# Kernel tuning notes

Measured on AMD Instinct MI355X. Metric: run time of the kernel, lower is better.

Reference implementation:

```python
import jax, jax.numpy as jnp
import numpy as np

N_NODES = 40000
IN_CH, HID_CH, OUT_CH = 128, 128, 64
N_EDGES = 640000
N_LABEL = 200000


def gcn_conv(x, edge_index, W, b):
    """PyG-style GCNConv: x' = D^{-1/2}(A+I)D^{-1/2} (x W) + b."""
    n = x.shape[0]
    loops = jnp.arange(n, dtype=edge_index.dtype)
    src = jnp.concatenate([edge_index[0], loops])  # [E+N]
    dst = jnp.concatenate([edge_index[1], loops])  # [E+N]
    deg = jax.ops.segment_sum(jnp.ones_like(dst, dtype=x.dtype), dst, num_segments=n)
    dinv = jnp.where(deg > 0, jax.lax.rsqrt(deg), 0.0)
    norm = dinv[src] * dinv[dst]                   # [E+N]
    h = x @ W                                      # [n, out]
    msg = h[src] * norm[:, None]                   # gather + scale
    agg = jax.ops.segment_sum(msg, dst, num_segments=n)
    return agg + b


def setup_inputs() -> dict:
    key = jax.random.key(0)
    k = jax.random.split(key, 8)
    x = jax.random.normal(k[0], (N_NODES, IN_CH), dtype=jnp.float32)
    edge_index = jax.random.randint(k[1], (2, N_EDGES), 0, N_NODES, dtype=jnp.int64)
    edge_label_index = jax.random.randint(k[2], (2, N_LABEL), 0, N_NODES, dtype=jnp.int64)
    s1 = 1.0 / np.sqrt(IN_CH)
    s2 = 1.0 / np.sqrt(HID_CH)
    W1 = jax.random.uniform(k[3], (IN_CH, HID_CH), jnp.float32, -s1, s1)
    b1 = jnp.zeros((HID_CH,), jnp.float32)
    W2 = jax.random.uniform(k[4], (HID_CH, OUT_CH), jnp.float32, -s2, s2)
    b2 = jnp.zeros((OUT_CH,), jnp.float32)
    return {"x": x, "edge_index": edge_index, "edge_label_index": edge_label_index,
            "W1": W1, "b1": b1, "W2": W2, "b2": b2}


def reference(x, edge_index, edge_label_index, W1, b1, W2, b2):
    # encode: conv1 -> relu -> conv2
    h = jax.nn.relu(gcn_conv(x, edge_index, W1, b1))
    z = gcn_conv(h, edge_index, W2, b2)            # [N, OUT_CH]
    # decode: dot-product score per candidate edge
    logits = jnp.sum(z[edge_label_index[0]] * z[edge_label_index[1]], axis=-1)
    return logits
```

## Files before the change

kernel.cpp:

```cpp
#include <hip/hip_runtime.h>
#include <hip/hip_bf16.h>

constexpr int IN_CH  = 128;
constexpr int HID_CH = 128;
constexpr int OUT_CH = 64;
constexpr int SCAN_CHUNK = 1024;

typedef __attribute__((ext_vector_type(8))) short bf16x8;
typedef __attribute__((ext_vector_type(4))) float f32x4;


__device__ inline unsigned short f2bf(float f) {
  __hip_bfloat16 h = __float2bfloat16(f);
  return *reinterpret_cast<unsigned short*>(&h);
}
__device__ inline unsigned pack_bf16x2(float lo, float hi) {
  return (unsigned)f2bf(lo) | ((unsigned)f2bf(hi) << 16);
}
__device__ inline float bf_lo(unsigned u) { return __uint_as_float(u << 16); }
__device__ inline float bf_hi(unsigned u) { return __uint_as_float(u & 0xffff0000u); }


__global__ __launch_bounds__(256) void k_zero(int* __restrict__ a, int n) {
  int i = (blockIdx.x * 256 + threadIdx.x) * 4;
  if (i + 3 < n) *(int4*)&a[i] = make_int4(0, 0, 0, 0);
  else for (int j = 0; j < 4 && i + j < n; ++j) a[i + j] = 0;
}


__global__ void k_count(const int* __restrict__ dst, int* __restrict__ cnt,
                        int* __restrict__ ord, int E) {
  int e = (blockIdx.x * blockDim.x + threadIdx.x) * 4;
  if (e + 3 < E) {
    int4 v = *(const int4*)&dst[e];
    int4 o;
    o.x = atomicAdd(&cnt[v.x], 1);
    o.y = atomicAdd(&cnt[v.y], 1);
    o.z = atomicAdd(&cnt[v.z], 1);
    o.w = atomicAdd(&cnt[v.w], 1);
    *(int4*)&ord[e] = o;
  } else {
    for (int j = 0; j < 4 && e + j < E; ++j) ord[e + j] = atomicAdd(&cnt[dst[e + j]], 1);
  }
}

__global__ __launch_bounds__(256) void k_scan_part(const int* __restrict__ cnt,
                                                   int* __restrict__ bsum,
                                                   float* __restrict__ dinv, int N) {
  int t = threadIdx.x;
  int base = blockIdx.x * SCAN_CHUNK + t * 4;
  int s = 0;
  if (base + 3 < N) {
    int4 v = *(const int4*)&cnt[base];
    s = v.x + v.y + v.z + v.w;
    float4 d;
    d.x = rsqrtf((float)v.x + 1.0f);
    d.y = rsqrtf((float)v.y + 1.0f);
    d.z = rsqrtf((float)v.z + 1.0f);
    d.w = rsqrtf((float)v.w + 1.0f);
    *(float4*)&dinv[base] = d;
  } else {
    for (int j = 0; j < 4; ++j)
      if (base + j < N) {
        int c = cnt[base + j];
        s += c;
        dinv[base + j] = rsqrtf((float)c + 1.0f);
      }
  }
  __shared__ int red[256];
  red[t] = s; __syncthreads();
  for (int off = 128; off; off >>= 1) {
    if (t < off) red[t] += red[t + off];
    __syncthreads();
  }
  if (t == 0) bsum[blockIdx.x] = red[0];
}

__global__ __launch_bounds__(256) void k_scan_fill(const int* __restrict__ cnt,
                                                   const int* __restrict__ bsum,
                                                   int* __restrict__ rowptr, int N, int E) {
  int t = threadIdx.x;
  int boff = 0;
  for (int i = 0; i < blockIdx.x; ++i) boff += bsum[i];
  int base = blockIdx.x * SCAN_CHUNK + t * 4;
  int v[4] = {0, 0, 0, 0};
  if (base + 3 < N) {
    int4 q = *(const int4*)&cnt[base];
    v[0] = q.x; v[1] = q.y; v[2] = q.z; v[3] = q.w;
  } else {
    for (int j = 0; j < 4; ++j) if (base + j < N) v[j] = cnt[base + j];
  }
  int mysum = v[0] + v[1] + v[2] + v[3];
  __shared__ int s[256];
  s[t] = mysum; __syncthreads();
  for (int off = 1; off < 256; off <<= 1) {
    int add = (t >= off) ? s[t - off] : 0;
    __syncthreads();
    s[t] += add;
    __syncthreads();
  }
  int run = boff + s[t] - mysum;
  for (int j = 0; j < 4; ++j) {
    if (base + j < N) rowptr[base + j] = run;
    run += v[j];
  }
  if (blockIdx.x == 0 && t == 0) rowptr[N] = E;
}

__global__ void k_fill(const int* __restrict__ src, const int* __restrict__ dst,
                       const int* __restrict__ ord, const int* __restrict__ rowptr,
                       int* __restrict__ col, int E) {
  int e0 = (blockIdx.x * blockDim.x + threadIdx.x) * 4;
  if (e0 >= E) return;
  if (e0 + 3 < E) {
    int4 sv = *(const int4*)&src[e0];
    int4 dv = *(const int4*)&dst[e0];
    int4 ov = *(const int4*)&ord[e0];
    col[rowptr[dv.x] + ov.x] = sv.x;
    col[rowptr[dv.y] + ov.y] = sv.y;
    col[rowptr[dv.z] + ov.z] = sv.z;
    col[rowptr[dv.w] + ov.w] = sv.w;
  } else {
    for (int j = 0; j < 4 && e0 + j < E; ++j)
      col[rowptr[dst[e0 + j]] + ord[e0 + j]] = src[e0 + j];
  }
}


template <int OUT, bool A_BF16>
__global__ __launch_bounds__(256) void k_gemm(const void* __restrict__ Xv,
                                              const float* __restrict__ W,
                                              const float* __restrict__ dinv,
                                              unsigned short* __restrict__ Y, int N) {
  constexpr int KD = 128;
  constexpr int NCG = OUT / 32;
  __shared__ unsigned short Wt[OUT * KD];
  int t = threadIdx.x;
  for (int i = t * 4; i < KD * OUT; i += 1024) {
    int k = i / OUT, c = i % OUT;
    float4 w4 = *(const float4*)&W[i];
    float wa[4] = {w4.x, w4.y, w4.z, w4.w};
#pragma unroll
    for (int j = 0; j < 4; ++j) {
      int colj = c + j;
      int byte = colj * (KD * 2) + k * 2;
      byte ^= ((colj & 7) << 4);
      *(unsigned short*)((char*)Wt + byte) = f2bf(wa[j]);
    }
  }
  __syncthreads();

  int w = t >> 6, l = t & 63;
  int lr = l & 15, kg = (l >> 4) * 8;
  int r = blockIdx.x * 64 + w * 16 + lr;
  bool valid = r < N;

  f32x4 acc[OUT / 16];
#pragma unroll
  for (int n = 0; n < OUT / 16; ++n) acc[n] = f32x4{0.f, 0.f, 0.f, 0.f};

#pragma unroll
  for (int kb = 0; kb < KD / 32; ++kb) {
    bf16x8 a = bf16x8{0, 0, 0, 0, 0, 0, 0, 0};
    if (valid) {
      if (A_BF16) {
        a = *(const bf16x8*)((const unsigned short*)Xv +
                             ((size_t)(kb >> 1) * N + r) * 64 + (kb & 1) * 32 + kg);
      } else {
        const float* xrow = (const float*)Xv + (size_t)r * KD + kb * 32 + kg;
        float4 x0 = *(const float4*)xrow;
        float4 x1 = *(const float4*)(xrow + 4);
        a[0] = (short)f2bf(x0.x); a[1] = (short)f2bf(x0.y);
        a[2] = (short)f2bf(x0.z); a[3] = (short)f2bf(x0.w);
        a[4] = (short)f2bf(x1.x); a[5] = (short)f2bf(x1.y);
        a[6] = (short)f2bf(x1.z); a[7] = (short)f2bf(x1.w);
      }
    }
#pragma unroll
    for (int n = 0; n < OUT / 16; ++n) {
      int col = n * 16 + lr;
      int byte = col * (KD * 2) + (kb * 32 + kg) * 2;
      byte ^= ((col & 7) << 4);
      bf16x8 b = *(const bf16x8*)((const char*)Wt + byte);
      acc[n] = __builtin_amdgcn_mfma_f32_16x16x32_bf16(a, b, acc[n], 0, 0, 0);
    }
  }

  int orow = blockIdx.x * 64 + w * 16 + (l >> 4) * 4;
  float dn[4];
#pragma unroll
  for (int i = 0; i < 4; ++i) dn[i] = (orow + i < N) ? dinv[orow + i] : 0.f;
#pragma unroll
  for (int i = 0; i < 4; ++i) {
    if (orow + i >= N) continue;
#pragma unroll
    for (int n = 0; n < OUT / 16; ++n)
      Y[((size_t)(n / NCG) * N + (orow + i)) * (OUT / 2) + (n % NCG) * 16 + lr] =
          f2bf(acc[n][i] * dn[i]);
  }
}


template <int CPU, bool RELU>
__global__ __launch_bounds__(256) void k_agg(const unsigned* __restrict__ T,
                                             const int* __restrict__ rowptr,
                                             const int* __restrict__ col,
                                             const float* __restrict__ dinv,
                                             const float* __restrict__ bias,
                                             unsigned* __restrict__ Out, int N) {
  constexpr int NPW = 64 / CPU;
  constexpr int NPB = 4 * NPW;
  int bid = blockIdx.x;
  int xcd = bid & 7, chunk = bid >> 3;
  int pass = xcd >> 2, sub = xcd & 3;
  int w = threadIdx.x >> 6, l = threadIdx.x & 63;
  int n = (chunk * 4 + sub) * NPB + w * NPW + l / CPU;
  if (n >= N) return;
  int cp = l % CPU;
  const unsigned* Tp = T + (size_t)pass * N * CPU;
  float dn = dinv[n];
  unsigned u0 = Tp[(size_t)n * CPU + cp];
  float ax = bf_lo(u0), ay = bf_hi(u0);
  int p = rowptr[n], pend = rowptr[n + 1];
  for (; p + 8 <= pend; p += 8) {
    int s[8]; unsigned g[8];
#pragma unroll
    for (int j = 0; j < 8; ++j) s[j] = __builtin_nontemporal_load(&col[p + j]);
#pragma unroll
    for (int j = 0; j < 8; ++j) g[j] = Tp[(size_t)s[j] * CPU + cp];
#pragma unroll
    for (int j = 0; j < 8; ++j) { ax += bf_lo(g[j]); ay += bf_hi(g[j]); }
  }
  if (p + 4 <= pend) {
    int s[4]; unsigned g[4];
#pragma unroll
    for (int j = 0; j < 4; ++j) s[j] = __builtin_nontemporal_load(&col[p + j]);
#pragma unroll
    for (int j = 0; j < 4; ++j) g[j] = Tp[(size_t)s[j] * CPU + cp];
#pragma unroll
    for (int j = 0; j < 4; ++j) { ax += bf_lo(g[j]); ay += bf_hi(g[j]); }
    p += 4;
  }
  for (; p < pend; ++p) {
    unsigned g = Tp[(size_t)__builtin_nontemporal_load(&col[p]) * CPU + cp];
    ax += bf_lo(g); ay += bf_hi(g);
  }
  float2 b2 = ((const float2*)bias)[pass * CPU + cp];
  float vx = dn * ax + b2.x, vy = dn * ay + b2.y;
  if (RELU) { vx = fmaxf(vx, 0.f); vy = fmaxf(vy, 0.f); }
  Out[(size_t)pass * N * CPU + (size_t)n * CPU + cp] = pack_bf16x2(vx, vy);
}


__global__ __launch_bounds__(256) void k_decode(const unsigned* __restrict__ Z,
                                                const int* __restrict__ ia,
                                                const int* __restrict__ ib,
                                                float* __restrict__ out, int N, int L) {
  int t = blockIdx.x * 256 + threadIdx.x;
  int i = t >> 3;
  if (i >= L) return;
  int e = t & 7;
  int a = ia[i], b = ib[i];
  size_t base = (size_t)(e >> 2) * N * 16 + (size_t)(e & 3) * 4;
  uint4 za = *(const uint4*)&Z[base + (size_t)a * 16];
  uint4 zb = *(const uint4*)&Z[base + (size_t)b * 16];
  float p = bf_lo(za.x) * bf_lo(zb.x) + bf_hi(za.x) * bf_hi(zb.x)
          + bf_lo(za.y) * bf_lo(zb.y) + bf_hi(za.y) * bf_hi(zb.y)
          + bf_lo(za.z) * bf_lo(zb.z) + bf_hi(za.z) * bf_hi(zb.z)
          + bf_lo(za.w) * bf_lo(zb.w) + bf_hi(za.w) * bf_hi(zb.w);
  p += __shfl_xor(p, 1);
  p += __shfl_xor(p, 2);
  p += __shfl_xor(p, 4);
  if (e == 0) out[i] = p;
}

extern "C" void kernel_launch(void* const* d_in, const int* in_sizes, int n_in,
                              void* d_out, int out_size, void* d_ws, size_t ws_size,
                              hipStream_t stream) {
  const float* x   = (const float*)d_in[0];
  const int*   ei  = (const int*)d_in[1];
  const int*   eli = (const int*)d_in[2];
  const float* W1  = (const float*)d_in[3];
  const float* b1  = (const float*)d_in[4];
  const float* W2  = (const float*)d_in[5];
  const float* b2  = (const float*)d_in[6];
  float* logits = (float*)d_out;

  int N = in_sizes[0] / IN_CH;
  int E = in_sizes[1] / 2;
  int L = in_sizes[2] / 2;
  const int* src = ei;
  const int* dst = ei + E;
  const int* la  = eli;
  const int* lb  = eli + L;

  char* ws = (char*)d_ws;
  size_t off = 0;
  auto alloc = [&](size_t bytes) {
    void* p = ws + off;
    off = (off + bytes + 255) & ~(size_t)255;
    return p;
  };
  int*      cnt    = (int*)alloc((size_t)N * 4);
  int*      rowptr = (int*)alloc((size_t)(N + 1) * 4);
  float*    dinv   = (float*)alloc((size_t)N * 4);
  int*      col    = (int*)alloc((size_t)E * 4);
  int*      ord    = (int*)alloc((size_t)E * 4);
  unsigned short* hsp  = (unsigned short*)alloc((size_t)N * HID_CH * 2);
  unsigned short* hrbp = (unsigned short*)alloc((size_t)N * HID_CH * 2);
  unsigned short* h2sp = (unsigned short*)alloc((size_t)N * OUT_CH * 2);
  unsigned short* zup  = (unsigned short*)alloc((size_t)N * OUT_CH * 2);
  int*      bsum   = (int*)alloc(256 * 4);

  const int TB = 256;
  int nscan = (N + SCAN_CHUNK - 1) / SCAN_CHUNK;
  k_zero<<<(N / 4 + TB - 1) / TB, TB, 0, stream>>>(cnt, N);
  k_count<<<(E / 4 + TB - 1) / TB, TB, 0, stream>>>(dst, cnt, ord, E);
  k_scan_part<<<nscan, 256, 0, stream>>>(cnt, bsum, dinv, N);
  k_scan_fill<<<nscan, 256, 0, stream>>>(cnt, bsum, rowptr, N, E);
  k_fill <<<(E / 4 + TB - 1) / TB, TB, 0, stream>>>(src, dst, ord, rowptr, col, E);

  k_gemm<HID_CH, false><<<(N + 63) / 64, 256, 0, stream>>>(x, W1, dinv, hsp, N);
  {
    int nchunk = (N + 8 * 4 - 1) / (8 * 4);
    k_agg<32, true><<<nchunk * 8, 256, 0, stream>>>(
        (const unsigned*)hsp, rowptr, col, dinv, b1, (unsigned*)hrbp, N);
  }

  k_gemm<OUT_CH, true><<<(N + 63) / 64, 256, 0, stream>>>(hrbp, W2, dinv, h2sp, N);
  {
    int nchunk = (N + 16 * 4 - 1) / (16 * 4);
    k_agg<16, false><<<nchunk * 8, 256, 0, stream>>>(
        (const unsigned*)h2sp, rowptr, col, dinv, b2, (unsigned*)zup, N);
  }

  k_decode<<<((size_t)L * 8 + 255) / 256, 256, 0, stream>>>(
      (const unsigned*)zup, la, lb, logits, N, L);
}
```

Baseline: 144.4 us.

## Split feature layout into 32-column slabs and make final embeddings row-contiguous

Layer-1 features now live in four 32-column bf16 slabs instead of two 64-column ones. Both aggregation kernels use 16 lanes per node, with passes spread across XCD-interleaved blocks, so each gathered row is a 64-byte segment. The second aggregation writes z row-contiguous with nontemporal stores, letting decode load one full 128-byte row per endpoint. This aims to improve per-XCD cache locality during gathers and to coalesce the decode reads, at the cost of more aggregation passes re-reading col/rowptr.

```diff
diff --git a/kernel.cpp b/kernel.cpp
--- a/kernel.cpp
+++ b/kernel.cpp
@@ -133,7 +133,6 @@
                                               const float* __restrict__ dinv,
                                               unsigned short* __restrict__ Y, int N) {
   constexpr int KD = 128;
-  constexpr int NCG = OUT / 32;
   __shared__ unsigned short Wt[OUT * KD];
   int t = threadIdx.x;
   for (int i = t * 4; i < KD * OUT; i += 1024) {
@@ -164,8 +163,7 @@
     bf16x8 a = bf16x8{0, 0, 0, 0, 0, 0, 0, 0};
     if (valid) {
       if (A_BF16) {
-        a = *(const bf16x8*)((const unsigned short*)Xv +
-                             ((size_t)(kb >> 1) * N + r) * 64 + (kb & 1) * 32 + kg);
+        a = *(const bf16x8*)((const unsigned short*)Xv + ((size_t)kb * N + r) * 32 + kg);
       } else {
         const float* xrow = (const float*)Xv + (size_t)r * KD + kb * 32 + kg;
         float4 x0 = *(const float4*)xrow;
@@ -195,31 +193,31 @@
     if (orow + i >= N) continue;
 #pragma unroll
     for (int n = 0; n < OUT / 16; ++n)
-      Y[((size_t)(n / NCG) * N + (orow + i)) * (OUT / 2) + (n % NCG) * 16 + lr] =
+      Y[((size_t)(n >> 1) * N + (orow + i)) * 32 + (n & 1) * 16 + lr] =
           f2bf(acc[n][i] * dn[i]);
   }
 }
 
 
-template <int CPU, bool RELU>
+template <int NPASS, bool RELU, bool CONTIG_OUT>
 __global__ __launch_bounds__(256) void k_agg(const unsigned* __restrict__ T,
                                              const int* __restrict__ rowptr,
                                              const int* __restrict__ col,
                                              const float* __restrict__ dinv,
                                              const float* __restrict__ bias,
                                              unsigned* __restrict__ Out, int N) {
-  constexpr int NPW = 64 / CPU;
-  constexpr int NPB = 4 * NPW;
+  constexpr int SUBS = 8 / NPASS;
+  constexpr int NPB  = 16;
   int bid = blockIdx.x;
   int xcd = bid & 7, chunk = bid >> 3;
-  int pass = xcd >> 2, sub = xcd & 3;
+  int pass = xcd / SUBS, sub = xcd % SUBS;
   int w = threadIdx.x >> 6, l = threadIdx.x & 63;
-  int n = (chunk * 4 + sub) * NPB + w * NPW + l / CPU;
+  int n = (chunk * SUBS + sub) * NPB + w * 4 + (l >> 4);
   if (n >= N) return;
-  int cp = l % CPU;
-  const unsigned* Tp = T + (size_t)pass * N * CPU;
+  int cp = l & 15;
+  const unsigned* Tp = T + (size_t)pass * N * 16;
   float dn = dinv[n];
-  unsigned u0 = Tp[(size_t)n * CPU + cp];
+  unsigned u0 = Tp[(size_t)n * 16 + cp];
   float ax = bf_lo(u0), ay = bf_hi(u0);
   int p = rowptr[n], pend = rowptr[n + 1];
   for (; p + 8 <= pend; p += 8) {
@@ -227,7 +225,7 @@
 #pragma unroll
     for (int j = 0; j < 8; ++j) s[j] = __builtin_nontemporal_load(&col[p + j]);
 #pragma unroll
-    for (int j = 0; j < 8; ++j) g[j] = Tp[(size_t)s[j] * CPU + cp];
+    for (int j = 0; j < 8; ++j) g[j] = Tp[(size_t)s[j] * 16 + cp];
 #pragma unroll
     for (int j = 0; j < 8; ++j) { ax += bf_lo(g[j]); ay += bf_hi(g[j]); }
   }
@@ -236,34 +234,36 @@
 #pragma unroll
     for (int j = 0; j < 4; ++j) s[j] = __builtin_nontemporal_load(&col[p + j]);
 #pragma unroll
-    for (int j = 0; j < 4; ++j) g[j] = Tp[(size_t)s[j] * CPU + cp];
+    for (int j = 0; j < 4; ++j) g[j] = Tp[(size_t)s[j] * 16 + cp];
 #pragma unroll
     for (int j = 0; j < 4; ++j) { ax += bf_lo(g[j]); ay += bf_hi(g[j]); }
     p += 4;
   }
   for (; p < pend; ++p) {
-    unsigned g = Tp[(size_t)__builtin_nontemporal_load(&col[p]) * CPU + cp];
+    unsigned g = Tp[(size_t)__builtin_nontemporal_load(&col[p]) * 16 + cp];
     ax += bf_lo(g); ay += bf_hi(g);
   }
-  float2 b2 = ((const float2*)bias)[pass * CPU + cp];
+  float2 b2 = ((const float2*)bias)[pass * 16 + cp];
   float vx = dn * ax + b2.x, vy = dn * ay + b2.y;
   if (RELU) { vx = fmaxf(vx, 0.f); vy = fmaxf(vy, 0.f); }
-  Out[(size_t)pass * N * CPU + (size_t)n * CPU + cp] = pack_bf16x2(vx, vy);
-}
-
-
-__global__ __launch_bounds__(256) void k_decode(const unsigned* __restrict__ Z,
+  unsigned ov = pack_bf16x2(vx, vy);
+  size_t oi = CONTIG_OUT ? ((size_t)n * (NPASS * 16) + (size_t)pass * 16 + cp)
+                         : (((size_t)pass * N + n) * 16 + cp);
+  __builtin_nontemporal_store(ov, &Out[oi]);
+}
+
+
+__global__ __launch_bounds__(256) void k_decode(const uint4* __restrict__ Z,
                                                 const int* __restrict__ ia,
                                                 const int* __restrict__ ib,
-                                                float* __restrict__ out, int N, int L) {
+                                                float* __restrict__ out, int L) {
   int t = blockIdx.x * 256 + threadIdx.x;
   int i = t >> 3;
   if (i >= L) return;
   int e = t & 7;
   int a = ia[i], b = ib[i];
-  size_t base = (size_t)(e >> 2) * N * 16 + (size_t)(e & 3) * 4;
-  uint4 za = *(const uint4*)&Z[base + (size_t)a * 16];
-  uint4 zb = *(const uint4*)&Z[base + (size_t)b * 16];
+  uint4 za = Z[(size_t)a * 8 + e];
+  uint4 zb = Z[(size_t)b * 8 + e];
   float p = bf_lo(za.x) * bf_lo(zb.x) + bf_hi(za.x) * bf_hi(zb.x)
           + bf_lo(za.y) * bf_lo(zb.y) + bf_hi(za.y) * bf_hi(zb.y)
           + bf_lo(za.z) * bf_lo(zb.z) + bf_hi(za.z) * bf_hi(zb.z)
@@ -321,19 +321,13 @@
   k_fill <<<(E / 4 + TB - 1) / TB, TB, 0, stream>>>(src, dst, ord, rowptr, col, E);
 
   k_gemm<HID_CH, false><<<(N + 63) / 64, 256, 0, stream>>>(x, W1, dinv, hsp, N);
-  {
-    int nchunk = (N + 8 * 4 - 1) / (8 * 4);
-    k_agg<32, true><<<nchunk * 8, 256, 0, stream>>>(
-        (const unsigned*)hsp, rowptr, col, dinv, b1, (unsigned*)hrbp, N);
-  }
+  k_agg<4, true, false><<<((N + 31) / 32) * 8, 256, 0, stream>>>(
+      (const unsigned*)hsp, rowptr, col, dinv, b1, (unsigned*)hrbp, N);
 
   k_gemm<OUT_CH, true><<<(N + 63) / 64, 256, 0, stream>>>(hrbp, W2, dinv, h2sp, N);
-  {
-    int nchunk = (N + 16 * 4 - 1) / (16 * 4);
-    k_agg<16, false><<<nchunk * 8, 256, 0, stream>>>(
-        (const unsigned*)h2sp, rowptr, col, dinv, b2, (unsigned*)zup, N);
-  }
+  k_agg<2, false, true><<<((N + 63) / 64) * 8, 256, 0, stream>>>(
+      (const unsigned*)h2sp, rowptr, col, dinv, b2, (unsigned*)zup, N);
 
   k_decode<<<((size_t)L * 8 + 255) / 256, 256, 0, stream>>>(
-      (const unsigned*)zup, la, lb, logits, N, L);
-}
+      (const uint4*)zup, la, lb, logits, L);
+}
```

Measured after the change: 149.1 us. 1.03x slower.
